# Kernel tuning notes

Measured on AMD Instinct MI355X. Metric: run time of the kernel, lower is better.

The kernel has to match this reference:

```python
import jax, jax.numpy as jnp
import numpy as np
from functools import partial

N_QUBITS = 8
DEPTH = 2
DIM = 2 ** N_QUBITS


@jax.checkpoint
def quantum_expval(angles):
    """Batched statevector sim of the PennyLane circuit.

    angles: [B, n_qubits] real. Circuit (repeated DEPTH times, same angles
    each layer, matching params.repeat(1, depth, 1)):
      RX(angles[w]) on every wire, then CNOT(w, w+1) chain.
    Returns <Z_0> per sample, shape [B].
    """
    B = angles.shape[0]
    c = jnp.cos(angles * 0.5).astype(jnp.complex64)
    s = jnp.sin(angles * 0.5).astype(jnp.complex64)
    state = jnp.zeros((B, DIM), jnp.complex64).at[:, 0].set(1.0)
    for _ in range(DEPTH):
        for w in range(N_QUBITS):
            # wire 0 is the most-significant bit (PennyLane convention)
            st = state.reshape(B, 2 ** w, 2, DIM // 2 ** (w + 1))
            cw = c[:, w][:, None, None]
            sw = s[:, w][:, None, None]
            a0, a1 = st[:, :, 0], st[:, :, 1]
            state = jnp.stack([cw * a0 - 1j * sw * a1,
                               -1j * sw * a0 + cw * a1], axis=2).reshape(B, DIM)
        for w in range(N_QUBITS - 1):
            # CNOT(control=w, target=w+1): flip target amplitudes when control=1
            st = state.reshape(B, 2 ** w, 2, 2, DIM // 2 ** (w + 2))
            flipped = st[:, :, 1, ::-1, :]
            state = jnp.concatenate([st[:, :, 0:1], flipped[:, :, None]], axis=2).reshape(B, DIM)
    p = jnp.real(state * jnp.conj(state)).reshape(B, 2, DIM // 2)
    return (p[:, 0].sum(-1) - p[:, 1].sum(-1)).astype(angles.dtype)


def qgate(combined, Wl, bl, Wq, bq):
    h = combined @ Wl.T + bl          # [B, hidden]
    ang = h @ Wq.T + bq               # [B, n_qubits]
    return quantum_expval(ang)        # [B]


def setup_inputs() -> dict:
    T, B, I, H, Q = 256, 256, 256, 256, N_QUBITS
    key = jax.random.key(0)
    ks = jax.random.split(key, 17)
    sc_l = 1.0 / np.sqrt(I + H)
    sc_q = 1.0 / np.sqrt(H)
    d = {"inputs": jax.random.normal(ks[0], (T, B, I), jnp.float32)}
    names = ["f", "i", "u", "o"]
    for j, n in enumerate(names):
        d[f"W{n}"] = jax.random.normal(ks[1 + j], (H, I + H), jnp.float32) * sc_l
        d[f"b{n}"] = jnp.zeros((H,), jnp.float32)
        d[f"W{n}q"] = jax.random.normal(ks[5 + j], (Q, H), jnp.float32) * sc_q
        d[f"b{n}q"] = jnp.zeros((Q,), jnp.float32)
    return d


def reference(inputs, Wf, bf, Wfq, bfq, Wi, bi, Wiq, biq,
              Wu, bu, Wuq, buq, Wo, bo, Woq, boq):
    T, B, _ = inputs.shape
    H = Wf.shape[0]
    h0 = jnp.zeros((B, H), inputs.dtype)
    c0 = jnp.zeros((B, H), inputs.dtype)

    def step(carry, x):
        hx, cx = carry
        comb = jnp.concatenate([x, hx], axis=1)          # [B, I+H]
        f = jax.nn.sigmoid(qgate(comb, Wf, bf, Wfq, bfq))[:, None]
        i = jax.nn.sigmoid(qgate(comb, Wi, bi, Wiq, biq))[:, None]
        g = jnp.tanh(qgate(comb, Wu, bu, Wuq, buq))[:, None]
        o = jax.nn.sigmoid(qgate(comb, Wo, bo, Woq, boq))[:, None]
        cx = f * cx + i * g
        hx = o * jnp.tanh(cx)
        return (hx, cx), hx

    (hx, cx), outputs = jax.lax.scan(step, (h0, c0), inputs)
    return outputs, (hx, cx)
```

## Files before the change

kernel.cpp:

```cpp
#include <hip/hip_runtime.h>

#define T_DIM 256
#define B_DIM 256
#define I_DIM 256
#define H_DIM 256
#define COMB  512
#define JCH   16
#define CHUNK 16
#define WARM  12
#define NSMAX (WARM + CHUNK)
#define NCH   (T_DIM / CHUNK)
#define REPS  64
#define RPB   2
#define FGRID (NCH * REPS / RPB)

typedef float f32x4 __attribute__((ext_vector_type(4)));

#define OFF_W    0
#define OFF_PS   1024
#define OFF_BETA 1056

__global__ __launch_bounds__(512) void k_w1(
    const float* W0, const float* Q0, const float* B0, const float* q0,
    const float* W1, const float* Q1, const float* B1, const float* q1,
    const float* W2, const float* Q2, const float* B2, const float* q2,
    const float* W3, const float* Q3, const float* B3, const float* q3,
    float* __restrict__ ws) {
  const float* W[4] = {W0, W1, W2, W3};
  const float* Q[4] = {Q0, Q1, Q2, Q3};
  const float* Bv[4] = {B0, B1, B2, B3};
  const float* qv[4] = {q0, q1, q2, q3};
  const int g = blockIdx.x >> 4, jc = blockIdx.x & (JCH - 1);
  const int tid = threadIdx.x;
  const int jj = tid & 31;
  const int ks = tid >> 5;
  const int j0 = jc * 32;
  const float* Wg = W[g];
  const float* Qg = Q[g];

  float acc = 0.f;
#pragma unroll
  for (int kk = 0; kk < 16; ++kk) {
    const int k = ks * 16 + kk;
    acc = fmaf(Qg[k], Wg[(size_t)k * COMB + j0 + jj], acc);
  }

  __shared__ float red[512];
  red[tid] = acc;
  __syncthreads();
  for (int s = 256; s >= 32; s >>= 1) {
    if (tid < s) red[tid] += red[tid + s];
    __syncthreads();
  }

  if (jc < 8) {
    if (tid < 32) ws[OFF_W + g * I_DIM + j0 + tid] = red[tid];
  } else {
    if (tid < 16) red[tid] += red[tid + 16];
    __syncthreads();
    if (tid < 8) red[tid] += red[tid + 8];
    __syncthreads();
    if (tid < 4) red[tid] += red[tid + 4];
    __syncthreads();
    if (tid < 2) red[tid] += red[tid + 2];
    __syncthreads();
    if (tid == 0) ws[OFF_PS + g * 8 + (jc - 8)] = red[0] + red[1];
  }

  if (jc == 0) {
    __syncthreads();
    red[tid] = (tid < H_DIM) ? Qg[tid] * Bv[g][tid] : 0.f;
    __syncthreads();
    for (int s = 256; s > 0; s >>= 1) {
      if (tid < s) red[tid] += red[tid + s];
      __syncthreads();
    }
    if (tid == 0) ws[OFF_BETA + g] = red[0] + qv[g][0];
  }
}

#define C0S 0.6224593312f
#define C1S 0.1175018561f
#define C2S (-0.0071946125f)
#define C3S (-0.0020074354f)
#define C4S 0.0002728000f

#define G0T 0.4621171573f
#define G1T 0.3932238600f
#define G2T (-0.0908577800f)
#define G3T (-0.0117749000f)
#define G4T 0.0102923100f
#define G5T (-0.0008507100f)

__device__ __forceinline__ float poly_sig(float u) {
  return fmaf(u, fmaf(u, fmaf(u, fmaf(u, C4S, C3S), C2S), C1S), C0S);
}
__device__ __forceinline__ float poly_tanhE(float u) {
  return fmaf(u, fmaf(u, fmaf(u, fmaf(u, fmaf(u, G5T, G4T), G3T), G2T), G1T), G0T);
}
__device__ __forceinline__ float pade_tanh(float x) {
  const float y = x * x;
  const float num = fmaf(y, fmaf(y, 1.0f, 105.0f), 945.0f);
  const float den = fmaf(y, fmaf(y, 15.0f, 420.0f), 945.0f);
  return x * num * __builtin_amdgcn_rcpf(den);
}

__global__ __launch_bounds__(256) void k_fused(const float* __restrict__ x,
                                               const float* __restrict__ ws,
                                               float* __restrict__ out) {
  const int bid = blockIdx.x, tid = threadIdx.x;

  __shared__ f32x4 wx4[4 * 64];
  __shared__ f32x4 a_lds[NSMAX][4];
  __shared__ float lds_h[CHUNK][4];
  __shared__ float lds_hc[2][4];

  reinterpret_cast<float*>(wx4)[tid] = ws[OFF_W + tid];
  reinterpret_cast<float*>(wx4)[tid + 256] = ws[OFF_W + tid + 256];
  reinterpret_cast<float*>(wx4)[tid + 512] = ws[OFF_W + tid + 512];
  reinterpret_cast<float*>(wx4)[tid + 768] = ws[OFF_W + tid + 768];

  float sg0 = 0.f, sg1 = 0.f, sg2 = 0.f, sg3 = 0.f;
#pragma unroll
  for (int p = 0; p < 8; ++p) {
    sg0 += ws[OFF_PS + 0 * 8 + p];
    sg1 += ws[OFF_PS + 1 * 8 + p];
    sg2 += ws[OFF_PS + 2 * 8 + p];
    sg3 += ws[OFF_PS + 3 * 8 + p];
  }
  sg0 *= 2.f; sg1 *= 2.f; sg2 *= 2.f; sg3 *= 2.f;
  const float bt0 = ws[OFF_BETA + 0], bt1 = ws[OFF_BETA + 1];
  const float bt2 = ws[OFF_BETA + 2], bt3 = ws[OFF_BETA + 3];
  __syncthreads();

#pragma unroll
  for (int item = 0; item < RPB; ++item) {
    const int wid = bid + item * FGRID;
    const int c = wid >> 6;
    const int rep = wid & (REPS - 1);
    const int t0 = c * CHUNK;
    const int w0 = (t0 > WARM) ? (t0 - WARM) : 0;
    const int NS = t0 + CHUNK - w0;

    const int npairs = NS * 2;
    if (tid < npairs) {
      const int riA = tid, riB = tid + npairs;
      const int rowA = (w0 + (riA >> 2)) * B_DIM + rep * 4 + (riA & 3);
      const int rowB = (w0 + (riB >> 2)) * B_DIM + rep * 4 + (riB & 3);
      const f32x4* xrA =
          reinterpret_cast<const f32x4*>(x + (size_t)rowA * I_DIM);
      const f32x4* xrB =
          reinterpret_cast<const f32x4*>(x + (size_t)rowB * I_DIM);
      float a0 = 0.f, a1 = 0.f, a2 = 0.f, a3 = 0.f;
      float b0 = 0.f, b1 = 0.f, b2 = 0.f, b3 = 0.f;
#pragma unroll 4
      for (int r = 0; r < 16; ++r) {
        f32x4 xa[4], xb[4];
#pragma unroll
        for (int q = 0; q < 4; ++q) xa[q] = xrA[r * 4 + q];
#pragma unroll
        for (int q = 0; q < 4; ++q) xb[q] = xrB[r * 4 + q];
#pragma unroll
        for (int q = 0; q < 4; ++q) {
          const f32x4 w0v = wx4[0 * 64 + r * 4 + q];
          const f32x4 w1v = wx4[1 * 64 + r * 4 + q];
          const f32x4 w2v = wx4[2 * 64 + r * 4 + q];
          const f32x4 w3v = wx4[3 * 64 + r * 4 + q];
          const f32x4 va = xa[q], vb = xb[q];
          a0 = fmaf(va.x, w0v.x, fmaf(va.y, w0v.y, fmaf(va.z, w0v.z, fmaf(va.w, w0v.w, a0))));
          a1 = fmaf(va.x, w1v.x, fmaf(va.y, w1v.y, fmaf(va.z, w1v.z, fmaf(va.w, w1v.w, a1))));
          a2 = fmaf(va.x, w2v.x, fmaf(va.y, w2v.y, fmaf(va.z, w2v.z, fmaf(va.w, w2v.w, a2))));
          a3 = fmaf(va.x, w3v.x, fmaf(va.y, w3v.y, fmaf(va.z, w3v.z, fmaf(va.w, w3v.w, a3))));
          b0 = fmaf(vb.x, w0v.x, fmaf(vb.y, w0v.y, fmaf(vb.z, w0v.z, fmaf(vb.w, w0v.w, b0))));
          b1 = fmaf(vb.x, w1v.x, fmaf(vb.y, w1v.y, fmaf(vb.z, w1v.z, fmaf(vb.w, w1v.w, b1))));
          b2 = fmaf(vb.x, w2v.x, fmaf(vb.y, w2v.y, fmaf(vb.z, w2v.z, fmaf(vb.w, w2v.w, b2))));
          b3 = fmaf(vb.x, w3v.x, fmaf(vb.y, w3v.y, fmaf(vb.z, w3v.z, fmaf(vb.w, w3v.w, b3))));
        }
      }
      a_lds[riA >> 2][riA & 3] = f32x4{2.f * (a0 + bt0), 2.f * (a1 + bt1),
                                       2.f * (a2 + bt2), 2.f * (a3 + bt3)};
      a_lds[riB >> 2][riB & 3] = f32x4{2.f * (b0 + bt0), 2.f * (b1 + bt1),
                                       2.f * (b2 + bt2), 2.f * (b3 + bt3)};
    }
    __syncthreads();

    if (tid < 4) {
      float C = 0.f, Hs = 0.f;
      const int kofs = NS - CHUNK;
      f32x4 nxt = a_lds[0][tid];
      for (int ts = 0; ts < NS; ++ts) {
        const f32x4 a = nxt;
        if (ts + 1 < NS) nxt = a_lds[ts + 1][tid];
        const float uf = __cosf(fmaf(Hs, sg0, a.x));
        const float ui = __cosf(fmaf(Hs, sg1, a.y));
        const float uu = __cosf(fmaf(Hs, sg2, a.z));
        const float uo = __cosf(fmaf(Hs, sg3, a.w));
        const float f = poly_sig(uf);
        const float i = poly_sig(ui);
        const float g = poly_tanhE(uu);
        const float o = poly_sig(uo);
        C = fmaf(f, C, i * g);
        Hs = o * pade_tanh(C);
        if (ts >= kofs) lds_h[ts - kofs][tid] = Hs;
      }
      lds_hc[0][tid] = Hs;
      lds_hc[1][tid] = C;
    }
    __syncthreads();

    f32x4* o4 = reinterpret_cast<f32x4*>(out);
#pragma unroll
    for (int it = 0; it < 16; ++it) {
      const int idx = it * 256 + tid;
      const int ts = idx >> 8;
      const int rem = idx & 255;
      const int bb = rem >> 6;
      const int f4 = rem & 63;
      const float v = lds_h[ts][bb];
      o4[((size_t)((t0 + ts) * B_DIM + rep * 4 + bb)) * 64 + f4] =
          f32x4{v, v, v, v};
    }
    if (c == NCH - 1) {
      const size_t N1 = (size_t)T_DIM * B_DIM * (H_DIM / 4);
#pragma unroll
      for (int it = 0; it < 2; ++it) {
        const int idx = it * 256 + tid;
        const int arr = idx >> 8;
        const int rem = idx & 255;
        const int bb = rem >> 6;
        const int f4 = rem & 63;
        const float v = (arr == 0) ? lds_hc[0][bb] : lds_hc[1][bb];
        o4[N1 + (size_t)arr * B_DIM * 64 + ((size_t)(rep * 4 + bb)) * 64 +
           f4] = f32x4{v, v, v, v};
      }
    }
  }
}

extern "C" void kernel_launch(void* const* d_in, const int* in_sizes, int n_in,
                              void* d_out, int out_size, void* d_ws,
                              size_t ws_size, hipStream_t stream) {
  const float* x = (const float*)d_in[0];
  const float* Wf = (const float*)d_in[1];
  const float* bf = (const float*)d_in[2];
  const float* Wfq = (const float*)d_in[3];
  const float* bfq = (const float*)d_in[4];
  const float* Wi = (const float*)d_in[5];
  const float* bi = (const float*)d_in[6];
  const float* Wiq = (const float*)d_in[7];
  const float* biq = (const float*)d_in[8];
  const float* Wu = (const float*)d_in[9];
  const float* bu = (const float*)d_in[10];
  const float* Wuq = (const float*)d_in[11];
  const float* buq = (const float*)d_in[12];
  const float* Wo = (const float*)d_in[13];
  const float* bo = (const float*)d_in[14];
  const float* Woq = (const float*)d_in[15];
  const float* boq = (const float*)d_in[16];

  float* ws = (float*)d_ws;
  float* out = (float*)d_out;

  k_w1<<<4 * JCH, 512, 0, stream>>>(Wf, Wfq, bf, bfq, Wi, Wiq, bi, biq, Wu,
                                    Wuq, bu, buq, Wo, Woq, bo, boq, ws);
  k_fused<<<FGRID, 256, 0, stream>>>(x, ws, out);
}
```

Measured before the change: 45.24 us.

## Overlap serial scan of one work item with projection and writes of another

Each block's two work items are restructured into a software pipeline with double-buffered LDS. Wave 0 runs the serial LSTM scan for item 0 while waves 1-3 compute the input projection for item 1. The scan for item 1 then overlaps with the output writes for item 0. The projection now uses one row per thread on 192 threads instead of two rows per thread, and the writes run on fewer threads. The aim is to hide the latency-bound single-wave scan behind memory and compute work.

```diff
diff --git a/kernel.cpp b/kernel.cpp
--- a/kernel.cpp
+++ b/kernel.cpp
@@ -11,8 +11,7 @@
 #define NSMAX (WARM + CHUNK)
 #define NCH   (T_DIM / CHUNK)
 #define REPS  64
-#define RPB   2
-#define FGRID (NCH * REPS / RPB)
+#define FGRID 512
 
 typedef float f32x4 __attribute__((ext_vector_type(4)));
 
@@ -105,15 +104,22 @@
   return x * num * __builtin_amdgcn_rcpf(den);
 }
 
+#define GEO(wid, c, rep, t0, w0v_, NS)              \
+  const int c = (wid) >> 6;                         \
+  const int rep = (wid) & (REPS - 1);               \
+  const int t0 = c * CHUNK;                         \
+  const int w0v_ = (t0 > WARM) ? (t0 - WARM) : 0;   \
+  const int NS = t0 + CHUNK - w0v_;
+
 __global__ __launch_bounds__(256) void k_fused(const float* __restrict__ x,
                                                const float* __restrict__ ws,
                                                float* __restrict__ out) {
   const int bid = blockIdx.x, tid = threadIdx.x;
 
   __shared__ f32x4 wx4[4 * 64];
-  __shared__ f32x4 a_lds[NSMAX][4];
-  __shared__ float lds_h[CHUNK][4];
-  __shared__ float lds_hc[2][4];
+  __shared__ f32x4 a_lds[2][NSMAX][4];
+  __shared__ float lds_h[2][CHUNK][4];
+  __shared__ float lds_hc[2][2][4];
 
   reinterpret_cast<float*>(wx4)[tid] = ws[OFF_W + tid];
   reinterpret_cast<float*>(wx4)[tid + 256] = ws[OFF_W + tid + 256];
@@ -133,108 +139,112 @@
   const float bt2 = ws[OFF_BETA + 2], bt3 = ws[OFF_BETA + 3];
   __syncthreads();
 
-#pragma unroll
-  for (int item = 0; item < RPB; ++item) {
-    const int wid = bid + item * FGRID;
-    const int c = wid >> 6;
-    const int rep = wid & (REPS - 1);
-    const int t0 = c * CHUNK;
-    const int w0 = (t0 > WARM) ? (t0 - WARM) : 0;
-    const int NS = t0 + CHUNK - w0;
-
-    const int npairs = NS * 2;
-    if (tid < npairs) {
-      const int riA = tid, riB = tid + npairs;
-      const int rowA = (w0 + (riA >> 2)) * B_DIM + rep * 4 + (riA & 3);
-      const int rowB = (w0 + (riB >> 2)) * B_DIM + rep * 4 + (riB & 3);
-      const f32x4* xrA =
-          reinterpret_cast<const f32x4*>(x + (size_t)rowA * I_DIM);
-      const f32x4* xrB =
-          reinterpret_cast<const f32x4*>(x + (size_t)rowB * I_DIM);
-      float a0 = 0.f, a1 = 0.f, a2 = 0.f, a3 = 0.f;
-      float b0 = 0.f, b1 = 0.f, b2 = 0.f, b3 = 0.f;
-#pragma unroll 4
-      for (int r = 0; r < 16; ++r) {
-        f32x4 xa[4], xb[4];
-#pragma unroll
-        for (int q = 0; q < 4; ++q) xa[q] = xrA[r * 4 + q];
-#pragma unroll
-        for (int q = 0; q < 4; ++q) xb[q] = xrB[r * 4 + q];
-#pragma unroll
-        for (int q = 0; q < 4; ++q) {
-          const f32x4 w0v = wx4[0 * 64 + r * 4 + q];
-          const f32x4 w1v = wx4[1 * 64 + r * 4 + q];
-          const f32x4 w2v = wx4[2 * 64 + r * 4 + q];
-          const f32x4 w3v = wx4[3 * 64 + r * 4 + q];
-          const f32x4 va = xa[q], vb = xb[q];
-          a0 = fmaf(va.x, w0v.x, fmaf(va.y, w0v.y, fmaf(va.z, w0v.z, fmaf(va.w, w0v.w, a0))));
-          a1 = fmaf(va.x, w1v.x, fmaf(va.y, w1v.y, fmaf(va.z, w1v.z, fmaf(va.w, w1v.w, a1))));
-          a2 = fmaf(va.x, w2v.x, fmaf(va.y, w2v.y, fmaf(va.z, w2v.z, fmaf(va.w, w2v.w, a2))));
-          a3 = fmaf(va.x, w3v.x, fmaf(va.y, w3v.y, fmaf(va.z, w3v.z, fmaf(va.w, w3v.w, a3))));
-          b0 = fmaf(vb.x, w0v.x, fmaf(vb.y, w0v.y, fmaf(vb.z, w0v.z, fmaf(vb.w, w0v.w, b0))));
-          b1 = fmaf(vb.x, w1v.x, fmaf(vb.y, w1v.y, fmaf(vb.z, w1v.z, fmaf(vb.w, w1v.w, b1))));
-          b2 = fmaf(vb.x, w2v.x, fmaf(vb.y, w2v.y, fmaf(vb.z, w2v.z, fmaf(vb.w, w2v.w, b2))));
-          b3 = fmaf(vb.x, w3v.x, fmaf(vb.y, w3v.y, fmaf(vb.z, w3v.z, fmaf(vb.w, w3v.w, b3))));
-        }
-      }
-      a_lds[riA >> 2][riA & 3] = f32x4{2.f * (a0 + bt0), 2.f * (a1 + bt1),
-                                       2.f * (a2 + bt2), 2.f * (a3 + bt3)};
-      a_lds[riB >> 2][riB & 3] = f32x4{2.f * (b0 + bt0), 2.f * (b1 + bt1),
-                                       2.f * (b2 + bt2), 2.f * (b3 + bt3)};
-    }
-    __syncthreads();
-
-    if (tid < 4) {
-      float C = 0.f, Hs = 0.f;
-      const int kofs = NS - CHUNK;
-      f32x4 nxt = a_lds[0][tid];
-      for (int ts = 0; ts < NS; ++ts) {
-        const f32x4 a = nxt;
-        if (ts + 1 < NS) nxt = a_lds[ts + 1][tid];
-        const float uf = __cosf(fmaf(Hs, sg0, a.x));
-        const float ui = __cosf(fmaf(Hs, sg1, a.y));
-        const float uu = __cosf(fmaf(Hs, sg2, a.z));
-        const float uo = __cosf(fmaf(Hs, sg3, a.w));
-        const float f = poly_sig(uf);
-        const float i = poly_sig(ui);
-        const float g = poly_tanhE(uu);
-        const float o = poly_sig(uo);
-        C = fmaf(f, C, i * g);
-        Hs = o * pade_tanh(C);
-        if (ts >= kofs) lds_h[ts - kofs][tid] = Hs;
-      }
-      lds_hc[0][tid] = Hs;
-      lds_hc[1][tid] = C;
-    }
-    __syncthreads();
-
-    f32x4* o4 = reinterpret_cast<f32x4*>(out);
-#pragma unroll
-    for (int it = 0; it < 16; ++it) {
-      const int idx = it * 256 + tid;
-      const int ts = idx >> 8;
-      const int rem = idx & 255;
-      const int bb = rem >> 6;
-      const int f4 = rem & 63;
-      const float v = lds_h[ts][bb];
-      o4[((size_t)((t0 + ts) * B_DIM + rep * 4 + bb)) * 64 + f4] =
-          f32x4{v, v, v, v};
-    }
-    if (c == NCH - 1) {
-      const size_t N1 = (size_t)T_DIM * B_DIM * (H_DIM / 4);
-#pragma unroll
-      for (int it = 0; it < 2; ++it) {
-        const int idx = it * 256 + tid;
-        const int arr = idx >> 8;
-        const int rem = idx & 255;
-        const int bb = rem >> 6;
-        const int f4 = rem & 63;
-        const float v = (arr == 0) ? lds_hc[0][bb] : lds_hc[1][bb];
-        o4[N1 + (size_t)arr * B_DIM * 64 + ((size_t)(rep * 4 + bb)) * 64 +
-           f4] = f32x4{v, v, v, v};
-      }
-    }
-  }
+  const int wid0 = bid, wid1 = bid + FGRID;
+
+#define PHASE1(wid, par)                                                      \
+  {                                                                           \
+    GEO(wid, c_, rep_, t0_, w0_, NS_)                                         \
+    const int w = tid - 64;                                                   \
+    if (w >= 0 && w < NS_ * 4) {                                              \
+      const int ts_ = w >> 2, bb_ = w & 3;                                    \
+      const int row_ = (w0_ + ts_) * B_DIM + rep_ * 4 + bb_;                  \
+      const f32x4* xr_ =                                                      \
+          reinterpret_cast<const f32x4*>(x + (size_t)row_ * I_DIM);           \
+      float p0 = 0.f, p1 = 0.f, p2 = 0.f, p3 = 0.f;                           \
+      _Pragma("unroll 4") for (int r = 0; r < 16; ++r) {                      \
+        f32x4 xq[4];                                                          \
+        _Pragma("unroll") for (int q = 0; q < 4; ++q) xq[q] = xr_[r * 4 + q]; \
+        _Pragma("unroll") for (int q = 0; q < 4; ++q) {                       \
+          const f32x4 xv = xq[q];                                             \
+          const f32x4 w0v = wx4[0 * 64 + r * 4 + q];                          \
+          const f32x4 w1v = wx4[1 * 64 + r * 4 + q];                          \
+          const f32x4 w2v = wx4[2 * 64 + r * 4 + q];                          \
+          const f32x4 w3v = wx4[3 * 64 + r * 4 + q];                          \
+          p0 = fmaf(xv.x, w0v.x, fmaf(xv.y, w0v.y, fmaf(xv.z, w0v.z, fmaf(xv.w, w0v.w, p0)))); \
+          p1 = fmaf(xv.x, w1v.x, fmaf(xv.y, w1v.y, fmaf(xv.z, w1v.z, fmaf(xv.w, w1v.w, p1)))); \
+          p2 = fmaf(xv.x, w2v.x, fmaf(xv.y, w2v.y, fmaf(xv.z, w2v.z, fmaf(xv.w, w2v.w, p2)))); \
+          p3 = fmaf(xv.x, w3v.x, fmaf(xv.y, w3v.y, fmaf(xv.z, w3v.z, fmaf(xv.w, w3v.w, p3)))); \
+        }                                                                     \
+      }                                                                       \
+      a_lds[par][ts_][bb_] = f32x4{2.f * (p0 + bt0), 2.f * (p1 + bt1),        \
+                                   2.f * (p2 + bt2), 2.f * (p3 + bt3)};       \
+    }                                                                         \
+  }
+
+#define SCAN(wid, par)                                                        \
+  {                                                                           \
+    GEO(wid, c_, rep_, t0_, w0_, NS_)                                         \
+    float C = 0.f, Hs = 0.f;                                                  \
+    const int kofs = NS_ - CHUNK;                                             \
+    f32x4 nxt = a_lds[par][0][tid];                                           \
+    for (int ts = 0; ts < NS_; ++ts) {                                        \
+      const f32x4 a = nxt;                                                    \
+      if (ts + 1 < NS_) nxt = a_lds[par][ts + 1][tid];                        \
+      const float uf = __cosf(fmaf(Hs, sg0, a.x));                            \
+      const float ui = __cosf(fmaf(Hs, sg1, a.y));                            \
+      const float uu = __cosf(fmaf(Hs, sg2, a.z));                            \
+      const float uo = __cosf(fmaf(Hs, sg3, a.w));                            \
+      const float f = poly_sig(uf);                                           \
+      const float i = poly_sig(ui);                                           \
+      const float g = poly_tanhE(uu);                                         \
+      const float o = poly_sig(uo);                                           \
+      C = fmaf(f, C, i * g);                                                  \
+      Hs = o * pade_tanh(C);                                                  \
+      if (ts >= kofs) lds_h[par][ts - kofs][tid] = Hs;                        \
+    }                                                                         \
+    lds_hc[par][0][tid] = Hs;                                                 \
+    lds_hc[par][1][tid] = C;                                                  \
+  }
+
+#define WRITE(wid, par, widx, nw)                                             \
+  {                                                                           \
+    GEO(wid, c_, rep_, t0_, w0_, NS_)                                         \
+    f32x4* o4 = reinterpret_cast<f32x4*>(out);                                \
+    for (int idx = (widx); idx < 4096; idx += (nw)) {                         \
+      const int ts = idx >> 8;                                                \
+      const int rem = idx & 255;                                              \
+      const int bb = rem >> 6;                                                \
+      const int f4 = rem & 63;                                                \
+      const float v = lds_h[par][ts][bb];                                     \
+      o4[((size_t)((t0_ + ts) * B_DIM + rep_ * 4 + bb)) * 64 + f4] =          \
+          f32x4{v, v, v, v};                                                  \
+    }                                                                         \
+    if (c_ == NCH - 1) {                                                      \
+      const size_t N1 = (size_t)T_DIM * B_DIM * (H_DIM / 4);                  \
+      for (int idx = (widx); idx < 512; idx += (nw)) {                        \
+        const int arr = idx >> 8;                                             \
+        const int rem = idx & 255;                                            \
+        const int bb = rem >> 6;                                              \
+        const int f4 = rem & 63;                                              \
+        const float v = (arr == 0) ? lds_hc[par][0][bb] : lds_hc[par][1][bb]; \
+        o4[N1 + (size_t)arr * B_DIM * 64 +                                    \
+           ((size_t)(rep_ * 4 + bb)) * 64 + f4] = f32x4{v, v, v, v};          \
+      }                                                                       \
+    }                                                                         \
+  }
+
+  PHASE1(wid0, 0);
+  __syncthreads();
+
+  if (tid >= 64) {
+    PHASE1(wid1, 1);
+  } else if (tid < 4) {
+    SCAN(wid0, 0);
+  }
+  __syncthreads();
+
+  if (tid < 4) {
+    SCAN(wid1, 1);
+  } else if (tid >= 64) {
+    WRITE(wid0, 0, tid - 64, 192);
+  }
+  __syncthreads();
+
+  WRITE(wid1, 1, tid, 256);
+
+#undef PHASE1
+#undef SCAN
+#undef WRITE
 }
 
 extern "C" void kernel_launch(void* const* d_in, const int* in_sizes, int n_in,
```

Result: faster. 37.68 us (-16.7%).
